# Optimization experiments

Hardware: AMD Instinct MI355X
Metric: run time of the kernel (lower is better)

## Reference

```python
import jax, jax.numpy as jnp
import numpy as np
import math

H = 2048; NH = 16; HD = 128; E = 8; K = 2; F = 8192; CAP_F = 1.25
B = 2; S = 2048

def _layernorm(x, scale, bias, eps=1e-5):
    m = jnp.mean(x, axis=-1, keepdims=True)
    v = jnp.var(x, axis=-1, keepdims=True)
    return (x - m) * jax.lax.rsqrt(v + eps) * scale + bias

def _rope(x):
    # x: [B, S, NH, HD]; half-split RoPE, theta=10000
    hd = x.shape[-1]
    pos = jnp.arange(x.shape[1], dtype=jnp.float32)
    freqs = 1.0 / (10000.0 ** (jnp.arange(0, hd // 2, dtype=jnp.float32) / (hd // 2)))
    ang = pos[:, None] * freqs[None, :]              # [S, HD/2]
    cos = jnp.cos(ang)[None, :, None, :]
    sin = jnp.sin(ang)[None, :, None, :]
    x1, x2 = jnp.split(x, 2, axis=-1)
    return jnp.concatenate([x1 * cos - x2 * sin, x1 * sin + x2 * cos], axis=-1)

def setup_inputs() -> dict:
    key = jax.random.key(0)
    ks = jax.random.split(key, 16)
    std = 0.02
    inp = {
        'hidden_states': jax.random.normal(ks[0], (B, S, H), jnp.float32),
        'attention_mask': jnp.ones((B, S), jnp.int32),
        'ln1_scale': jnp.ones((H,), jnp.float32), 'ln1_bias': jnp.zeros((H,), jnp.float32),
        'ln2_scale': jnp.ones((H,), jnp.float32), 'ln2_bias': jnp.zeros((H,), jnp.float32),
        'Wq': jax.random.normal(ks[1], (H, NH * HD), jnp.float32) * std,
        'Wk': jax.random.normal(ks[2], (H, NH * HD), jnp.float32) * std,
        'Wv': jax.random.normal(ks[3], (H, NH * HD), jnp.float32) * std,
        'Wo': jax.random.normal(ks[4], (NH * HD, H), jnp.float32) * std,
        'Wg': jax.random.normal(ks[5], (H, H), jnp.float32) * std,
        'bg': jnp.zeros((H,), jnp.float32),
        'ls_attn': jnp.full((H,), 0.1, jnp.float32),
        'ls_moe': jnp.full((H,), 0.1, jnp.float32),
        'router_w': jax.random.normal(ks[6], (H, E), jnp.float32) * std,
        'W1': jax.random.normal(ks[7], (E, H, F), jnp.float32) * std,
        'b1': jnp.zeros((E, F), jnp.float32),
        'W2': jax.random.normal(ks[8], (E, F, H), jnp.float32) * std,
        'b2': jnp.zeros((E, H), jnp.float32),
    }
    return inp

def _forward(hidden_states, attention_mask, ln1_scale, ln1_bias, ln2_scale, ln2_bias,
             Wq, Wk, Wv, Wo, Wg, bg, ls_attn, ls_moe, router_w, W1, b1, W2, b2):
    b, s, h = hidden_states.shape
    # ---- pre-norm MLA attention + residual ----
    xn = _layernorm(hidden_states, ln1_scale, ln1_bias)
    q = (xn @ Wq).reshape(b, s, NH, HD)
    k = (xn @ Wk).reshape(b, s, NH, HD)
    v = (xn @ Wv).reshape(b, s, NH, HD)
    q = _rope(q); k = _rope(k)
    scores = jnp.einsum('bqhd,bkhd->bhqk', q, k) / math.sqrt(HD)
    causal = jnp.tril(jnp.ones((s, s), bool))
    mask = causal[None, None, :, :] & (attention_mask[:, None, None, :] > 0)
    scores = jnp.where(mask, scores, -1e9)
    attn = jax.nn.softmax(scores, axis=-1)
    ctx = jnp.einsum('bhqk,bkhd->bqhd', attn, v).reshape(b, s, NH * HD)
    attn_out = ctx @ Wo
    attn_out = attn_out * jax.nn.sigmoid(xn @ Wg + bg)   # output gating
    attn_out = attn_out * ls_attn                         # layer scale
    hidden_states = hidden_states + attn_out
    # ---- pre-norm MoE FFN + residual ----
    xn2 = _layernorm(hidden_states, ln2_scale, ln2_bias)
    T = b * s
    x = xn2.reshape(T, h)
    logits = (x @ router_w).astype(jnp.float32)           # [T, E]
    probs = jax.nn.softmax(logits, axis=-1)
    gates, idx = jax.lax.top_k(probs, K)                  # [T, K]
    gates = gates / jnp.sum(gates, axis=-1, keepdims=True)
    cap = int(math.ceil(T * K / E * CAP_F))               # expert capacity
    e_flat = idx.reshape(T * K)
    g_flat = gates.reshape(T * K)
    oh = jax.nn.one_hot(e_flat, E, dtype=jnp.int32)       # [TK, E]
    pos = jnp.sum(jnp.cumsum(oh, axis=0) * oh, axis=-1) - 1
    keep = (pos < cap).astype(x.dtype)
    pos_c = jnp.clip(pos, 0, cap - 1)
    x_rep = jnp.repeat(x, K, axis=0)                      # [TK, H]
    buf = jnp.zeros((E, cap, h), x.dtype).at[e_flat, pos_c].add(x_rep * keep[:, None])
    hmid = jax.nn.gelu(jnp.einsum('ech,ehf->ecf', buf, W1) + b1[:, None, :])
    obuf = jnp.einsum('ecf,efh->ech', hmid, W2) + b2[:, None, :]
    tok = obuf[e_flat, pos_c] * (keep * g_flat)[:, None]  # [TK, H]
    moe_out = tok.reshape(T, K, h).sum(axis=1).reshape(b, s, h)
    moe_out = moe_out * ls_moe
    return hidden_states + moe_out

def reference(hidden_states, attention_mask, ln1_scale, ln1_bias, ln2_scale, ln2_bias,
              Wq, Wk, Wv, Wo, Wg, bg, ls_attn, ls_moe, router_w, W1, b1, W2, b2):
    return _forward(hidden_states, attention_mask, ln1_scale, ln1_bias, ln2_scale, ln2_bias,
                    Wq, Wk, Wv, Wo, Wg, bg, ls_attn, ls_moe, router_w, W1, b1, W2, b2)
```

## Files before the change

### kernel.cpp

```cpp
#include <hip/hip_runtime.h>
#include <hip/hip_fp16.h>

typedef _Float16 f16;
typedef _Float16 half8 __attribute__((ext_vector_type(8)));
typedef float floatx4 __attribute__((ext_vector_type(4)));

constexpr int kH  = 2048;
constexpr int kS  = 2048;
constexpr int kB  = 2;
constexpr int kT  = kB * kS;
constexpr int kNH = 16;
constexpr int kHD = 128;
constexpr int kE  = 8;
constexpr int kF  = 8192;
constexpr int kCAP = 1280;
constexpr int kTK = kT * 2;

__device__ __forceinline__ void gload16(const void* g, void* lds_) {
  __builtin_amdgcn_global_load_lds((const __attribute__((address_space(1))) void*)g,
                                   (__attribute__((address_space(3))) void*)lds_,
                                   16, 0, 0);
}

__global__ __launch_bounds__(256) void transpose_cvt(
    const float* __restrict__ src, f16* __restrict__ dst,
    int ldS, int ldD, long sZ, long dZ)
{
  __shared__ float tile[64][65];
  src += (long)blockIdx.z * sZ;
  dst += (long)blockIdx.z * dZ;
  const int kb = blockIdx.y * 64, nb = blockIdx.x * 64;
  const int tx = threadIdx.x & 15, ty = threadIdx.x >> 4;
#pragma unroll
  for (int i = 0; i < 4; i++) {
    const int r = ty + i * 16;
    const float4 v = *(const float4*)&src[(long)(kb + r) * ldS + nb + tx * 4];
    tile[r][tx * 4 + 0] = v.x; tile[r][tx * 4 + 1] = v.y;
    tile[r][tx * 4 + 2] = v.z; tile[r][tx * 4 + 3] = v.w;
  }
  __syncthreads();
#pragma unroll
  for (int i = 0; i < 4; i++) {
    const int n = ty + i * 16;
    union { f16 h[4]; unsigned long long u; } pk;
#pragma unroll
    for (int j = 0; j < 4; j++) pk.h[j] = (f16)tile[tx * 4 + j][n];
    *(unsigned long long*)&dst[(long)(nb + n) * ldD + kb + tx * 4] = pk.u;
  }
}

__global__ __launch_bounds__(256) void ln_kernel(
    const float* __restrict__ x, const float* __restrict__ sc,
    const float* __restrict__ bi, f16* __restrict__ o16, float* __restrict__ o32)
{
  const long row = blockIdx.x;
  const float* xr = x + row * kH;
  const int t = threadIdx.x;
  const float4 u = ((const float4*)xr)[t * 2];
  const float4 v = ((const float4*)xr)[t * 2 + 1];
  float s = u.x + u.y + u.z + u.w + v.x + v.y + v.z + v.w;
  float q = u.x*u.x + u.y*u.y + u.z*u.z + u.w*u.w + v.x*v.x + v.y*v.y + v.z*v.z + v.w*v.w;
#pragma unroll
  for (int m = 1; m < 64; m <<= 1) { s += __shfl_xor(s, m); q += __shfl_xor(q, m); }
  __shared__ float red_s[4], red_q[4];
  const int w = t >> 6, l = t & 63;
  if (l == 0) { red_s[w] = s; red_q[w] = q; }
  __syncthreads();
  s = red_s[0] + red_s[1] + red_s[2] + red_s[3];
  q = red_q[0] + red_q[1] + red_q[2] + red_q[3];
  const float mean = s * (1.f / kH);
  const float var = q * (1.f / kH) - mean * mean;
  const float rstd = rsqrtf(var + 1e-5f);
  const int c = t * 8;
  const float vals[8] = {u.x, u.y, u.z, u.w, v.x, v.y, v.z, v.w};
#pragma unroll
  for (int j = 0; j < 8; j++) {
    const float y = (vals[j] - mean) * rstd * sc[c + j] + bi[c + j];
    o16[row * kH + c + j] = (f16)y;
    if (o32 != nullptr) o32[row * kH + c + j] = y;
  }
}

template <int EPI>
__global__ __launch_bounds__(256) void gemm_kernel(
    const f16* __restrict__ A, const f16* __restrict__ B, void* __restrict__ Cv,
    const float* __restrict__ bias, const int* __restrict__ rowCount,
    int M, int N, int K, long aZ, long bZ, long cZ, long biasZ)
{
  const int z = blockIdx.z;
  if (rowCount != nullptr && (int)(blockIdx.y * 128) >= rowCount[z]) return;
  __shared__ f16 As[128 * 64];
  __shared__ f16 Bs[128 * 64];
  A += (long)z * aZ;  B += (long)z * bZ;
  const int tid = threadIdx.x, w = tid >> 6, l = tid & 63;
  const int g = l >> 4, lr = l & 15;
  const long m0 = (long)blockIdx.y * 128, n0 = (long)blockIdx.x * 128;
  const int wm = (w >> 1) * 64, wn = (w & 1) * 64;
  floatx4 acc[4][4];
#pragma unroll
  for (int i = 0; i < 4; i++)
#pragma unroll
    for (int j = 0; j < 4; j++) acc[i][j] = floatx4{0.f, 0.f, 0.f, 0.f};
  const int lrow = l >> 3, lwb = (l & 7) * 16;
  const int nk = K >> 6;
  for (int kt = 0; kt < nk; kt++) {
    const long k0 = (long)kt * 64;
#pragma unroll
    for (int c = 0; c < 4; c++) {
      const int rbase = w * 32 + c * 8;
      const int row = rbase + lrow;
      const int srcoff = (lwb ^ ((row & 7) << 4)) >> 1;
      gload16(A + (m0 + row) * K + k0 + srcoff, As + rbase * 64);
      gload16(B + (n0 + row) * K + k0 + srcoff, Bs + rbase * 64);
    }
    asm volatile("s_waitcnt vmcnt(0)" ::: "memory");
    __syncthreads();
#pragma unroll
    for (int kc = 0; kc < 2; kc++) {
      half8 af[4], bf[4];
#pragma unroll
      for (int i = 0; i < 4; i++) {
        const int ra = wm + i * 16 + lr;
        af[i] = *(const half8*)((const char*)As + ra * 128 + ((kc * 64 + g * 16) ^ ((ra & 7) << 4)));
        const int rb = wn + i * 16 + lr;
        bf[i] = *(const half8*)((const char*)Bs + rb * 128 + ((kc * 64 + g * 16) ^ ((rb & 7) << 4)));
      }
#pragma unroll
      for (int mi = 0; mi < 4; mi++)
#pragma unroll
        for (int ni = 0; ni < 4; ni++)
          acc[mi][ni] = __builtin_amdgcn_mfma_f32_16x16x32_f16(af[mi], bf[ni], acc[mi][ni], 0, 0, 0);
    }
    __syncthreads();
  }
  const long crow = m0 + wm + g * 4;
  const long ccol = n0 + wn + lr;
#pragma unroll
  for (int mi = 0; mi < 4; mi++)
#pragma unroll
    for (int ni = 0; ni < 4; ni++)
#pragma unroll
      for (int j = 0; j < 4; j++) {
        const long r = crow + mi * 16 + j;
        const long c = ccol + ni * 16;
        float v = acc[mi][ni][j];
        if (EPI == 0) {
          ((float*)Cv)[(long)z * cZ + r * N + c] = v;
        } else {
          v += bias[(long)z * biasZ + c];
          ((f16*)Cv)[(long)z * cZ + r * N + c] = (f16)v;
        }
      }
}

#define STG(SRC, TILE, KC, PAR, MAT) { \
  const f16* s_ = (SRC) + (long)(TILE) * 64 + (KC) * 32; \
  char* d_ = lds + ((PAR) * 65536 + (MAT) * 32768 + (KC) * 16384) + ldsW; \
  gload16(s_, d_); \
  gload16(s_ + 128 * ldGl, d_ + 8192); }

#define MROW(MH, MM, AF) \
  acc[(MH)*4+(MM)][0] = __builtin_amdgcn_mfma_f32_16x16x32_f16(AF, bf0, acc[(MH)*4+(MM)][0], 0, 0, 0); \
  acc[(MH)*4+(MM)][1] = __builtin_amdgcn_mfma_f32_16x16x32_f16(AF, bf1, acc[(MH)*4+(MM)][1], 0, 0, 0); \
  acc[(MH)*4+(MM)][2] = __builtin_amdgcn_mfma_f32_16x16x32_f16(AF, bf2, acc[(MH)*4+(MM)][2], 0, 0, 0); \
  acc[(MH)*4+(MM)][3] = __builtin_amdgcn_mfma_f32_16x16x32_f16(AF, bf3, acc[(MH)*4+(MM)][3], 0, 0, 0);

#define PH(PAR, KC, MH, RB, STAGE_STMT, VM_STMT) { \
  const char* au_ = lds + ((PAR) * 65536 + (KC) * 16384); \
  const char* bu_ = lds + ((PAR) * 65536 + 32768 + (KC) * 16384); \
  af0 = *(const half8*)(au_ + afoff + (MH) * 4096 +    0); \
  af1 = *(const half8*)(au_ + afoff + (MH) * 4096 + 1024); \
  af2 = *(const half8*)(au_ + afoff + (MH) * 4096 + 2048); \
  af3 = *(const half8*)(au_ + afoff + (MH) * 4096 + 3072); \
  if (RB) { \
    bf0 = *(const half8*)(bu_ + bfoff +    0); \
    bf1 = *(const half8*)(bu_ + bfoff + 1024); \
    bf2 = *(const half8*)(bu_ + bfoff + 2048); \
    bf3 = *(const half8*)(bu_ + bfoff + 3072); \
  } \
  STAGE_STMT; \
  VM_STMT; \
  __builtin_amdgcn_sched_barrier(0); \
  __builtin_amdgcn_s_barrier(); \
  asm volatile("s_waitcnt lgkmcnt(0)" ::: "memory"); \
  __builtin_amdgcn_sched_barrier(0); \
  __builtin_amdgcn_s_setprio(1); \
  MROW(MH, 0, af0) MROW(MH, 1, af1) MROW(MH, 2, af2) MROW(MH, 3, af3) \
  __builtin_amdgcn_s_setprio(0); }

#define VM6 asm volatile("s_waitcnt vmcnt(6)" ::: "memory")
#define VM0 asm volatile("s_waitcnt vmcnt(0)" ::: "memory")
#define NOP (void)0

template <int EPI, bool SPLITK>
__global__ __launch_bounds__(512, 2) void gemm8p_kernel(
    const f16* __restrict__ A, const f16* __restrict__ B, void* __restrict__ Cv,
    const float* __restrict__ bias, const int* __restrict__ rowCount,
    int M, int N, int K, long ldA, long ldB, long aZ, long bZ, long cZ,
    long cZ2, long biasZ)
{
  const int z = blockIdx.z;
  const int ze = SPLITK ? (z >> 1) : z;
  if (rowCount != nullptr && (int)(blockIdx.y * 256) >= rowCount[ze]) return;
  __shared__ __align__(16) char lds[131072];
  const long khoff = SPLITK ? (long)(z & 1) * K : 0;
  A += (long)ze * aZ + khoff;  B += (long)ze * bZ + khoff;
  const int tid = threadIdx.x, w = tid >> 6, l = tid & 63;
  const int g = l >> 4, lr = l & 15;
  const long m0 = (long)blockIdx.y * 256, n0 = (long)blockIdx.x * 256;
  const int wm = (w >> 2) * 128, wn = (w & 3) * 64;

  floatx4 acc[8][4];
#pragma unroll
  for (int i = 0; i < 8; i++)
#pragma unroll
    for (int j = 0; j < 4; j++) acc[i][j] = floatx4{0.f, 0.f, 0.f, 0.f};

  const int swzS = ((l & 3) * 8) ^ (((l >> 3) & 3) << 3);
  const f16* aSrc;
  const f16* bSrc;
  long ldGl;
  {
    const int srow = w * 16 + (l >> 2);
    aSrc = A + (m0 + srow) * ldA + swzS;
    bSrc = B + (n0 + srow) * ldB + swzS;
  }
  ldGl = ldA;
  const int ldsW = w * 1024;
  const int rsw = (g * 16) ^ (((lr >> 1) & 3) << 4);
  const int afoff = wm * 64 + lr * 64 + rsw;
  const int bfoff = wn * 64 + lr * 64 + rsw;
  half8 af0, af1, af2, af3;
  half8 bf0 = half8{0}, bf1 = half8{0}, bf2 = half8{0}, bf3 = half8{0};

  STG(aSrc, 0, 0, 0, 0);
  STG(bSrc, 0, 0, 0, 1);
  STG(aSrc, 0, 1, 0, 0);
  STG(bSrc, 0, 1, 0, 1);
  STG(bSrc, 1, 0, 1, 1);
  STG(aSrc, 1, 0, 1, 0);
  STG(bSrc, 1, 1, 1, 1);
  VM6;
  __builtin_amdgcn_sched_barrier(0);
  __builtin_amdgcn_s_barrier();

  const int NI = K >> 7;
  for (int i = 0; i < NI - 1; i++) {
    const int t0 = 2 * i, t1 = 2 * i + 1;
    PH(0, 0, 0, 1, STG(aSrc, (t1),     1, 1, 0), NOP)
    PH(0, 0, 1, 0, STG(bSrc, (t0 + 2), 0, 0, 1), NOP)
    PH(0, 1, 0, 1, STG(aSrc, (t0 + 2), 0, 0, 0), NOP)
    PH(0, 1, 1, 0, STG(bSrc, (t0 + 2), 1, 0, 1), VM6)
    PH(1, 0, 0, 1, STG(aSrc, (t0 + 2), 1, 0, 0), NOP)
    PH(1, 0, 1, 0, STG(bSrc, (t1 + 2), 0, 1, 1), NOP)
    PH(1, 1, 0, 1, STG(aSrc, (t1 + 2), 0, 1, 0), NOP)
    PH(1, 1, 1, 0, STG(bSrc, (t1 + 2), 1, 1, 1), VM6)
  }
  {
    const int t1 = 2 * (NI - 1) + 1;
    PH(0, 0, 0, 1, STG(aSrc, (t1), 1, 1, 0), NOP)
    PH(0, 0, 1, 0, NOP, NOP)
    PH(0, 1, 0, 1, NOP, NOP)
    PH(0, 1, 1, 0, NOP, VM0)
    PH(1, 0, 0, 1, NOP, NOP)
    PH(1, 0, 1, 0, NOP, NOP)
    PH(1, 1, 0, 1, NOP, NOP)
    PH(1, 1, 1, 0, NOP, NOP)
  }

  const long crow = m0 + wm + g * 4;
  const long ccol = n0 + wn + lr;
  float* c32 = (float*)Cv + (long)ze * cZ + (SPLITK ? (long)(z & 1) * cZ2 : 0);
#pragma unroll
  for (int mi = 0; mi < 8; mi++)
#pragma unroll
    for (int ni = 0; ni < 4; ni++)
#pragma unroll
      for (int j = 0; j < 4; j++) {
        const long r = crow + mi * 16 + j;
        const long c = ccol + ni * 16;
        float v = acc[mi][ni][j];
        if (EPI == 0) {
          c32[r * N + c] = v;
        } else if (EPI == 2) {
          v += bias[(long)ze * biasZ + c];
          const float u2 = 1.5957691216057308f * (v + 0.044715f * v * v * v);
          const float sg = 1.f / (1.f + __expf(-u2));
          ((f16*)Cv)[(long)ze * cZ + r * N + c] = (f16)(v * sg);
        } else {
          v += bias[(long)ze * biasZ + c];
          ((f16*)Cv)[(long)ze * cZ + r * N + c] = (f16)v;
        }
      }
}
#undef STG
#undef MROW
#undef PH
#undef VM6
#undef VM0
#undef NOP

__global__ void rope_table_kernel(float* __restrict__ ct, float* __restrict__ st) {
  const int i = blockIdx.x * 256 + threadIdx.x;
  if (i >= kS * 64) return;
  const int s = i >> 6, f = i & 63;
  const double freq = exp(-0.14391156831212787 * (double)f);
  const double ang = (double)s * freq;
  ct[i] = (float)cos(ang);
  st[i] = (float)sin(ang);
}

__global__ __launch_bounds__(256) void rope_kernel(
    const float* __restrict__ q, const float* __restrict__ k,
    const float* __restrict__ ct, const float* __restrict__ st,
    f16* __restrict__ qr, f16* __restrict__ kr)
{
  const long t = blockIdx.x;
  const int s = (int)(t & (kS - 1)), b = (int)(t >> 11);
  for (int u = threadIdx.x; u < kNH * 64; u += 256) {
    const int h = u >> 6, i = u & 63;
    const float c = ct[s * 64 + i], sn = st[s * 64 + i];
    const long src = t * kH + h * kHD + i;
    const long dst = (((long)(b * kNH + h)) * kS + s) * kHD + i;
    float x1 = q[src], x2 = q[src + 64];
    qr[dst]      = (f16)((x1 * c - x2 * sn) * 0.08838834764831845f);
    qr[dst + 64] = (f16)((x1 * sn + x2 * c) * 0.08838834764831845f);
    x1 = k[src]; x2 = k[src + 64];
    kr[dst]      = (f16)(x1 * c - x2 * sn);
    kr[dst + 64] = (f16)(x1 * sn + x2 * c);
  }
}

__global__ __launch_bounds__(256) void attn_kernel(
    const f16* __restrict__ q_r, const f16* __restrict__ k_r,
    const f16* __restrict__ v_t, f16* __restrict__ ctx)
{
  __shared__ f16 Ks[64 * 128];
  __shared__ f16 Vs[128 * 64];
  __shared__ f16 Ps[4][1024];
  const int qt = blockIdx.x, h = blockIdx.y, b = blockIdx.z;
  const int bh = b * kNH + h;
  const int tid = threadIdx.x, w = tid >> 6, l = tid & 63;
  const int g = l >> 4, lr = l & 15;
  const long q0 = (long)qt * 64;
  const f16* qbase = q_r + ((long)bh * kS + q0 + w * 16 + lr) * kHD;
  half8 qf[4];
#pragma unroll
  for (int kc = 0; kc < 4; kc++) qf[kc] = *(const half8*)(qbase + kc * 32 + g * 8);
  floatx4 acc[8];
#pragma unroll
  for (int i = 0; i < 8; i++) acc[i] = floatx4{0.f, 0.f, 0.f, 0.f};
  float mrun[4], lrun[4];
#pragma unroll
  for (int j = 0; j < 4; j++) { mrun[j] = -1e30f; lrun[j] = 0.f; }
  f16* pw = Ps[w];

  for (int kt = 0; kt <= qt; kt++) {
    const long k0 = (long)kt * 64;
#pragma unroll
    for (int c = 0; c < 4; c++) {
      const int cc = w * 4 + c;
      const int row = cc * 4 + (l >> 4);
      const int wb = (l & 15) * 16;
      const int src = (wb ^ ((row & 7) << 4)) >> 1;
      gload16(k_r + ((long)bh * kS + k0 + row) * kHD + src, Ks + cc * 512);
    }
#pragma unroll
    for (int c = 0; c < 4; c++) {
      const int cc = w * 4 + c;
      const int row = cc * 8 + (l >> 3);
      const int wb = (l & 7) * 16;
      const int src = (wb ^ ((row & 7) << 4)) >> 1;
      gload16(v_t + ((long)bh * kHD + row) * kS + k0 + src, Vs + cc * 512);
    }
    asm volatile("s_waitcnt vmcnt(0)" ::: "memory");
    __syncthreads();

    floatx4 sfr[4];
#pragma unroll
    for (int f = 0; f < 4; f++) {
      floatx4 s4 = floatx4{0.f, 0.f, 0.f, 0.f};
      const int row = f * 16 + lr;
#pragma unroll
      for (int kc = 0; kc < 4; kc++) {
        const half8 kfq = *(const half8*)((const char*)Ks + row * 256 +
                            ((kc * 64 + g * 16) ^ ((row & 7) << 4)));
        s4 = __builtin_amdgcn_mfma_f32_16x16x32_f16(qf[kc], kfq, s4, 0, 0, 0);
      }
      sfr[f] = s4;
    }
    if (kt == qt) {
#pragma unroll
      for (int f = 0; f < 4; f++) {
        const int key = kt * 64 + f * 16 + lr;
#pragma unroll
        for (int j = 0; j < 4; j++) {
          const int qrow = qt * 64 + w * 16 + g * 4 + j;
          if (key > qrow) sfr[f][j] = -1e30f;
        }
      }
    }
    float al[4];
#pragma unroll
    for (int j = 0; j < 4; j++) {
      float pm = fmaxf(fmaxf(sfr[0][j], sfr[1][j]), fmaxf(sfr[2][j], sfr[3][j]));
      pm = fmaxf(pm, __shfl_xor(pm, 1)); pm = fmaxf(pm, __shfl_xor(pm, 2));
      pm = fmaxf(pm, __shfl_xor(pm, 4)); pm = fmaxf(pm, __shfl_xor(pm, 8));
      const float mn = fmaxf(mrun[j], pm);
      al[j] = __expf(mrun[j] - mn);
      mrun[j] = mn;
      float rs = 0.f;
#pragma unroll
      for (int f = 0; f < 4; f++) {
        const float p = __expf(sfr[f][j] - mn);
        sfr[f][j] = p; rs += p;
      }
      rs += __shfl_xor(rs, 1); rs += __shfl_xor(rs, 2);
      rs += __shfl_xor(rs, 4); rs += __shfl_xor(rs, 8);
      lrun[j] = lrun[j] * al[j] + rs;
    }
#pragma unroll
    for (int nf = 0; nf < 8; nf++)
#pragma unroll
      for (int j = 0; j < 4; j++) acc[nf][j] *= al[j];
#pragma unroll
    for (int f = 0; f < 4; f++)
#pragma unroll
      for (int j = 0; j < 4; j++) {
        const int row = g * 4 + j;
        const int byteoff = (row * 128 + (f * 16 + lr) * 2) ^ ((row & 7) << 4);
        *(f16*)((char*)pw + byteoff) = (f16)sfr[f][j];
      }
#pragma unroll
    for (int kc = 0; kc < 2; kc++) {
      const half8 pf = *(const half8*)((const char*)pw + lr * 128 +
                         ((kc * 64 + g * 16) ^ ((lr & 7) << 4)));
#pragma unroll
      for (int nf = 0; nf < 8; nf++) {
        const int vrow = nf * 16 + lr;
        const half8 vfr = *(const half8*)((const char*)Vs + vrow * 128 +
                            ((kc * 64 + g * 16) ^ ((vrow & 7) << 4)));
        acc[nf] = __builtin_amdgcn_mfma_f32_16x16x32_f16(pf, vfr, acc[nf], 0, 0, 0);
      }
    }
    __syncthreads();
  }
  const long orow = (long)b * kS + q0 + w * 16;
#pragma unroll
  for (int j = 0; j < 4; j++) {
    const float inv = 1.0f / lrun[j];
    const int r = g * 4 + j;
#pragma unroll
    for (int nf = 0; nf < 8; nf++)
      ctx[(orow + r) * kH + h * kHD + nf * 16 + lr] = (f16)(acc[nf][j] * inv);
  }
}

__global__ __launch_bounds__(256) void combine1_kernel(
    const float* __restrict__ hid, const float* __restrict__ alin,
    const float* __restrict__ glin, const float* __restrict__ bg,
    const float* __restrict__ ls, float* __restrict__ out)
{
  const long i = (long)blockIdx.x * 256 + threadIdx.x;
  const float4 hv = ((const float4*)hid)[i];
  const float4 av = ((const float4*)alin)[i];
  const float4 gv = ((const float4*)glin)[i];
  const int c = (int)(i & 511);
  const float4 lv = ((const float4*)ls)[c];
  const float4 bv = ((const float4*)bg)[c];
  float4 o;
  o.x = hv.x + lv.x * av.x / (1.f + __expf(-(gv.x + bv.x)));
  o.y = hv.y + lv.y * av.y / (1.f + __expf(-(gv.y + bv.y)));
  o.z = hv.z + lv.z * av.z / (1.f + __expf(-(gv.z + bv.z)));
  o.w = hv.w + lv.w * av.w / (1.f + __expf(-(gv.w + bv.w)));
  ((float4*)out)[i] = o;
}

__global__ __launch_bounds__(256) void router_kernel(
    const float* __restrict__ x, const float* __restrict__ rw,
    int* __restrict__ eidx, float* __restrict__ gates)
{
  const int t = blockIdx.x * 4 + (threadIdx.x >> 6);
  const int l = threadIdx.x & 63;
  const float* xr = x + (long)t * kH;
  float a[8] = {0.f, 0.f, 0.f, 0.f, 0.f, 0.f, 0.f, 0.f};
  for (int it = 0; it < kH / 64; it++) {
    const float xv = xr[it * 64 + l];
    const float* r = rw + (long)(it * 64 + l) * kE;
#pragma unroll
    for (int e = 0; e < 8; e++) a[e] += xv * r[e];
  }
#pragma unroll
  for (int e = 0; e < 8; e++)
#pragma unroll
    for (int m = 1; m < 64; m <<= 1) a[e] += __shfl_xor(a[e], m);
  if (l == 0) {
    float mx = a[0];
#pragma unroll
    for (int e = 1; e < 8; e++) mx = fmaxf(mx, a[e]);
    float p[8];
#pragma unroll
    for (int e = 0; e < 8; e++) p[e] = __expf(a[e] - mx);
    int i1 = 0; float v1 = p[0];
#pragma unroll
    for (int e = 1; e < 8; e++) if (p[e] > v1) { v1 = p[e]; i1 = e; }
    int i2 = -1; float v2 = -1.f;
#pragma unroll
    for (int e = 0; e < 8; e++) if (e != i1 && p[e] > v2) { v2 = p[e]; i2 = e; }
    const float inv = 1.f / (v1 + v2);
    eidx[t * 2] = i1; eidx[t * 2 + 1] = i2;
    gates[t * 2] = v1 * inv; gates[t * 2 + 1] = v2 * inv;
  }
}

__global__ void scan_kernel(const int* __restrict__ eidx, int* __restrict__ slot,
                            int* __restrict__ counts)
{
  const int l = threadIdx.x;
  int base[8] = {0, 0, 0, 0, 0, 0, 0, 0};
  const unsigned long long lt = (1ull << l) - 1ull;
  for (int it = 0; it < kTK / 64; it++) {
    const int i = it * 64 + l;
    const int e = eidx[i];
    int mypos = 0;
#pragma unroll
    for (int ex = 0; ex < 8; ex++) {
      const unsigned long long mk = __ballot(e == ex);
      if (e == ex) mypos = base[ex] + __popcll(mk & lt);
      base[ex] += __popcll(mk);
    }
    slot[i] = (mypos < kCAP) ? e * kCAP + mypos : -1;
  }
  if (l == 0) {
#pragma unroll
    for (int ex = 0; ex < 8; ex++) counts[ex] = min(base[ex], kCAP);
  }
}

__global__ __launch_bounds__(256) void scatter_kernel(
    const f16* __restrict__ xh, const int* __restrict__ slot, f16* __restrict__ buf)
{
  const int i = blockIdx.x;
  const int s = slot[i];
  if (s < 0) return;
  const long t = i >> 1;
  ((half8*)(buf + (long)s * kH))[threadIdx.x] =
      ((const half8*)(xh + t * kH))[threadIdx.x];
}

__global__ __launch_bounds__(256) void combine2_kernel(
    const float* __restrict__ hid2, const float* __restrict__ P0,
    const float* __restrict__ P1, const int* __restrict__ slot,
    const float* __restrict__ gates, const float* __restrict__ b2,
    const float* __restrict__ ls, float* __restrict__ out)
{
  const int t = blockIdx.x;
  const int c = threadIdx.x * 8;
  float m[8] = {0.f, 0.f, 0.f, 0.f, 0.f, 0.f, 0.f, 0.f};
#pragma unroll
  for (int ks = 0; ks < 2; ks++) {
    const int s = slot[t * 2 + ks];
    if (s < 0) continue;
    const float gte = gates[t * 2 + ks];
    const int e = s / kCAP;
    const long ro = (long)s * kH + c;
    const float4 p0a = *(const float4*)&P0[ro];
    const float4 p0b = *(const float4*)&P0[ro + 4];
    const float4 p1a = *(const float4*)&P1[ro];
    const float4 p1b = *(const float4*)&P1[ro + 4];
    const float4 ba = *(const float4*)&b2[e * kH + c];
    const float4 bb = *(const float4*)&b2[e * kH + c + 4];
    m[0] += gte * (p0a.x + p1a.x + ba.x);
    m[1] += gte * (p0a.y + p1a.y + ba.y);
    m[2] += gte * (p0a.z + p1a.z + ba.z);
    m[3] += gte * (p0a.w + p1a.w + ba.w);
    m[4] += gte * (p0b.x + p1b.x + bb.x);
    m[5] += gte * (p0b.y + p1b.y + bb.y);
    m[6] += gte * (p0b.z + p1b.z + bb.z);
    m[7] += gte * (p0b.w + p1b.w + bb.w);
  }
  const float* hp = hid2 + (long)t * kH + c;
  float* op = out + (long)t * kH + c;
#pragma unroll
  for (int j = 0; j < 8; j++) op[j] = hp[j] + ls[c + j] * m[j];
}

extern "C" void kernel_launch(void* const* d_in, const int* in_sizes, int n_in,
                              void* d_out, int out_size, void* d_ws, size_t ws_size,
                              hipStream_t stream)
{
  (void)in_sizes; (void)n_in;
  const float* hidden   = (const float*)d_in[0];
  const float* ln1s     = (const float*)d_in[2];
  const float* ln1b     = (const float*)d_in[3];
  const float* ln2s     = (const float*)d_in[4];
  const float* ln2b     = (const float*)d_in[5];
  const float* Wq       = (const float*)d_in[6];
  const float* Wk       = (const float*)d_in[7];
  const float* Wv       = (const float*)d_in[8];
  const float* Wo       = (const float*)d_in[9];
  const float* Wg       = (const float*)d_in[10];
  const float* bg       = (const float*)d_in[11];
  const float* ls_attn  = (const float*)d_in[12];
  const float* ls_moe   = (const float*)d_in[13];
  const float* router_w = (const float*)d_in[14];
  const float* W1       = (const float*)d_in[15];
  const float* b1       = (const float*)d_in[16];
  const float* W2       = (const float*)d_in[17];
  const float* b2       = (const float*)d_in[18];

  char* ws = (char*)d_ws;
  size_t off = 0;
  auto take = [&](size_t b) { size_t r = off; off += (b + 255) & ~(size_t)255; return r; };
  const size_t o_wT   = take(5ULL * kH * kH * 2);
  const size_t o_w1t  = take((size_t)kE * kF * kH * 2);
  const size_t o_w2t  = take((size_t)kE * kH * kF * 2);
  const size_t o_xn   = take((size_t)kT * kH * 2);
  const size_t o_qkvg = take(4ULL * kT * kH * 4);
  const size_t o_tab  = take(2ULL * kS * 64 * 4);
  const size_t o_qr   = take(3ULL * kT * kH * 2);
  const size_t o_ctx  = take((size_t)kT * kH * 2);
  const size_t o_h2   = take((size_t)kT * kH * 4);
  const size_t o_sm   = take(1 << 20);
  const size_t o_hmid = take((size_t)kE * kCAP * kF * 2);
  if (off > ws_size) { hipMemsetAsync(d_out, 0xFF, (size_t)out_size * 4, stream); return; }

  f16* wT    = (f16*)(ws + o_wT);
  f16* w1t   = (f16*)(ws + o_w1t);
  f16* w2t   = (f16*)(ws + o_w2t);
  f16* xn    = (f16*)(ws + o_xn);
  float* qf  = (float*)(ws + o_qkvg);
  float* kfp = qf + (size_t)kT * kH;
  float* vfp = kfp + (size_t)kT * kH;
  float* gfp = vfp + (size_t)kT * kH;
  float* tabc = (float*)(ws + o_tab);
  float* tabs = tabc + (size_t)kS * 64;
  f16* qr  = (f16*)(ws + o_qr);
  f16* kr  = qr + (size_t)kT * kH;
  f16* vt  = kr + (size_t)kT * kH;
  f16* ctx = (f16*)(ws + o_ctx);
  float* h2 = (float*)(ws + o_h2);
  int* eidx    = (int*)(ws + o_sm);
  float* gates = (float*)(ws + o_sm + 65536);
  int* slot    = (int*)(ws + o_sm + 131072);
  int* counts  = (int*)(ws + o_sm + 196608);
  f16* hmid = (f16*)(ws + o_hmid);
  float* attn_lin = qf;
  float* x2f = vfp;
  f16* x2h  = (f16*)(ws + o_qkvg + 1ULL * kT * kH * 4 + (size_t)kT * kH * 2);
  f16* buf  = qr;
  float* P0 = (float*)(ws + o_qkvg);
  float* P1 = (float*)(ws + o_w1t);
  const long pStride = (long)(P1 - P0);

  const long HH = (long)kH * kH;

  transpose_cvt<<<dim3(32, 32, 1), 256, 0, stream>>>(Wq, wT + 0 * HH, kH, kH, 0, 0);
  transpose_cvt<<<dim3(32, 32, 1), 256, 0, stream>>>(Wk, wT + 1 * HH, kH, kH, 0, 0);
  transpose_cvt<<<dim3(32, 32, 1), 256, 0, stream>>>(Wv, wT + 2 * HH, kH, kH, 0, 0);
  transpose_cvt<<<dim3(32, 32, 1), 256, 0, stream>>>(Wg, wT + 3 * HH, kH, kH, 0, 0);
  transpose_cvt<<<dim3(32, 32, 1), 256, 0, stream>>>(Wo, wT + 4 * HH, kH, kH, 0, 0);
  transpose_cvt<<<dim3(kF / 64, kH / 64, kE), 256, 0, stream>>>(
      W1, w1t, kF, kH, (long)kH * kF, (long)kF * kH);
  transpose_cvt<<<dim3(kH / 64, kF / 64, kE), 256, 0, stream>>>(
      W2, w2t, kH, kF, (long)kF * kH, (long)kH * kF);
  ln_kernel<<<kT, 256, 0, stream>>>(hidden, ln1s, ln1b, xn, nullptr);
  gemm8p_kernel<0, false><<<dim3(kH / 256, kT / 256, 4), 512, 0, stream>>>(
      xn, wT, qf, nullptr, nullptr, kT, kH, kH, kH, kH,
      0L, HH, (long)kT * kH, 0L, 0L);
  rope_table_kernel<<<(kS * 64 + 255) / 256, 256, 0, stream>>>(tabc, tabs);
  rope_kernel<<<kT, 256, 0, stream>>>(qf, kfp, tabc, tabs, qr, kr);
  for (int b = 0; b < kB; b++)
    transpose_cvt<<<dim3(kHD / 64, kS / 64, kNH), 256, 0, stream>>>(
        vfp + (size_t)b * kS * kH, vt + (size_t)b * kNH * kHD * kS,
        kH, kS, 128L, (long)kHD * kS);
  attn_kernel<<<dim3(kS / 64, kNH, kB), 256, 0, stream>>>(qr, kr, vt, ctx);
  gemm_kernel<0><<<dim3(kH / 128, kT / 128, 1), 256, 0, stream>>>(
      ctx, wT + 4 * HH, attn_lin, nullptr, nullptr, kT, kH, kH, 0L, 0L, 0L, 0L);
  combine1_kernel<<<(kT * kH / 4) / 256, 256, 0, stream>>>(
      hidden, attn_lin, gfp, bg, ls_attn, h2);
  ln_kernel<<<kT, 256, 0, stream>>>(h2, ln2s, ln2b, x2h, x2f);
  router_kernel<<<kT / 4, 256, 0, stream>>>(x2f, router_w, eidx, gates);
  scan_kernel<<<1, 64, 0, stream>>>(eidx, slot, counts);
  scatter_kernel<<<kTK, 256, 0, stream>>>(x2h, slot, buf);
  gemm8p_kernel<2, false><<<dim3(kF / 256, kCAP / 256, kE), 512, 0, stream>>>(
      buf, w1t, hmid, b1, counts, kCAP, kF, kH, kH, kH,
      (long)kCAP * kH, (long)kF * kH, (long)kCAP * kF, 0L, (long)kF);
  gemm8p_kernel<0, true><<<dim3(kH / 256, kCAP / 256, 2 * kE), 512, 0, stream>>>(
      hmid, w2t, P0, nullptr, counts, kCAP, kH, 4096, kF, kF,
      (long)kCAP * kF, (long)kH * kF, (long)kCAP * kH, pStride, 0L);
  combine2_kernel<<<kT, 256, 0, stream>>>(
      h2, P0, P1, slot, gates, b2, ls_moe, (float*)d_out);
}
```

Before: 1.692 ms.

## Add XCD-aware block remapping and finer-grained vmcnt waits in GEMM pipeline

Adds an xcd_remap helper that renumbers workgroups so consecutive logical tiles land on the same XCD, and applies it to the GEMM and attention kernels to improve L2 locality. The GEMM main loop swaps the coarse per-half vmcnt(6) waits for a vmcnt(10) wait in every phase, with a retuned drain in the tail. The intent is to keep more global->LDS loads in flight and to cut cache misses across XCDs. The remap assumes the total grid is divisible by 8, and the new wait counts must match the exact load issue order or stale LDS data could be read.

After: 1.635 ms. 1.04x faster.

```diff
diff --git a/kernel.cpp b/kernel.cpp
--- a/kernel.cpp
+++ b/kernel.cpp
@@ -20,6 +20,16 @@
   __builtin_amdgcn_global_load_lds((const __attribute__((address_space(1))) void*)g,
                                    (__attribute__((address_space(3))) void*)lds_,
                                    16, 0, 0);
+}
+
+__device__ __forceinline__ void xcd_remap(int& bx, int& by, int& bz) {
+  const int gx = gridDim.x, gy = gridDim.y;
+  const int nwg = gx * gy * gridDim.z;
+  int L = (bz * gy + by) * gx + bx;
+  L = (L & 7) * (nwg >> 3) + (L >> 3);
+  bz = L / (gx * gy);
+  const int r = L - bz * gx * gy;
+  by = r / gx;  bx = r - by * gx;
 }
 
 __global__ __launch_bounds__(256) void transpose_cvt(
@@ -188,8 +198,10 @@
   MROW(MH, 0, af0) MROW(MH, 1, af1) MROW(MH, 2, af2) MROW(MH, 3, af3) \
   __builtin_amdgcn_s_setprio(0); }
 
-#define VM6 asm volatile("s_waitcnt vmcnt(6)" ::: "memory")
-#define VM0 asm volatile("s_waitcnt vmcnt(0)" ::: "memory")
+#define VM10 asm volatile("s_waitcnt vmcnt(10)" ::: "memory")
+#define VM8  asm volatile("s_waitcnt vmcnt(8)" ::: "memory")
+#define VM4  asm volatile("s_waitcnt vmcnt(4)" ::: "memory")
+#define VM0  asm volatile("s_waitcnt vmcnt(0)" ::: "memory")
 #define NOP (void)0
 
 template <int EPI, bool SPLITK>
@@ -199,15 +211,17 @@
     int M, int N, int K, long ldA, long ldB, long aZ, long bZ, long cZ,
     long cZ2, long biasZ)
 {
-  const int z = blockIdx.z;
+  int bx = blockIdx.x, by = blockIdx.y, bz = blockIdx.z;
+  xcd_remap(bx, by, bz);
+  const int z = bz;
   const int ze = SPLITK ? (z >> 1) : z;
-  if (rowCount != nullptr && (int)(blockIdx.y * 256) >= rowCount[ze]) return;
+  if (rowCount != nullptr && (int)(by * 256) >= rowCount[ze]) return;
   __shared__ __align__(16) char lds[131072];
   const long khoff = SPLITK ? (long)(z & 1) * K : 0;
   A += (long)ze * aZ + khoff;  B += (long)ze * bZ + khoff;
   const int tid = threadIdx.x, w = tid >> 6, l = tid & 63;
   const int g = l >> 4, lr = l & 15;
-  const long m0 = (long)blockIdx.y * 256, n0 = (long)blockIdx.x * 256;
+  const long m0 = (long)by * 256, n0 = (long)bx * 256;
   const int wm = (w >> 2) * 128, wn = (w & 3) * 64;
 
   floatx4 acc[8][4];
@@ -240,29 +254,29 @@
   STG(bSrc, 1, 0, 1, 1);
   STG(aSrc, 1, 0, 1, 0);
   STG(bSrc, 1, 1, 1, 1);
-  VM6;
+  VM10;
   __builtin_amdgcn_sched_barrier(0);
   __builtin_amdgcn_s_barrier();
 
   const int NI = K >> 7;
   for (int i = 0; i < NI - 1; i++) {
     const int t0 = 2 * i, t1 = 2 * i + 1;
-    PH(0, 0, 0, 1, STG(aSrc, (t1),     1, 1, 0), NOP)
-    PH(0, 0, 1, 0, STG(bSrc, (t0 + 2), 0, 0, 1), NOP)
-    PH(0, 1, 0, 1, STG(aSrc, (t0 + 2), 0, 0, 0), NOP)
-    PH(0, 1, 1, 0, STG(bSrc, (t0 + 2), 1, 0, 1), VM6)
-    PH(1, 0, 0, 1, STG(aSrc, (t0 + 2), 1, 0, 0), NOP)
-    PH(1, 0, 1, 0, STG(bSrc, (t1 + 2), 0, 1, 1), NOP)
-    PH(1, 1, 0, 1, STG(aSrc, (t1 + 2), 0, 1, 0), NOP)
-    PH(1, 1, 1, 0, STG(bSrc, (t1 + 2), 1, 1, 1), VM6)
+    PH(0, 0, 0, 1, STG(aSrc, (t1),     1, 1, 0), VM10)
+    PH(0, 0, 1, 0, STG(bSrc, (t0 + 2), 0, 0, 1), VM10)
+    PH(0, 1, 0, 1, STG(aSrc, (t0 + 2), 0, 0, 0), VM10)
+    PH(0, 1, 1, 0, STG(bSrc, (t0 + 2), 1, 0, 1), VM10)
+    PH(1, 0, 0, 1, STG(aSrc, (t0 + 2), 1, 0, 0), VM10)
+    PH(1, 0, 1, 0, STG(bSrc, (t1 + 2), 0, 1, 1), VM10)
+    PH(1, 1, 0, 1, STG(aSrc, (t1 + 2), 0, 1, 0), VM10)
+    PH(1, 1, 1, 0, STG(bSrc, (t1 + 2), 1, 1, 1), VM10)
   }
   {
     const int t1 = 2 * (NI - 1) + 1;
-    PH(0, 0, 0, 1, STG(aSrc, (t1), 1, 1, 0), NOP)
+    PH(0, 0, 0, 1, STG(aSrc, (t1), 1, 1, 0), VM8)
     PH(0, 0, 1, 0, NOP, NOP)
-    PH(0, 1, 0, 1, NOP, NOP)
-    PH(0, 1, 1, 0, NOP, VM0)
-    PH(1, 0, 0, 1, NOP, NOP)
+    PH(0, 1, 0, 1, NOP, VM4)
+    PH(0, 1, 1, 0, NOP, NOP)
+    PH(1, 0, 0, 1, NOP, VM0)
     PH(1, 0, 1, 0, NOP, NOP)
     PH(1, 1, 0, 1, NOP, NOP)
     PH(1, 1, 1, 0, NOP, NOP)
@@ -296,7 +310,9 @@
 #undef STG
 #undef MROW
 #undef PH
-#undef VM6
+#undef VM10
+#undef VM8
+#undef VM4
 #undef VM0
 #undef NOP
 
@@ -338,7 +354,8 @@
   __shared__ f16 Ks[64 * 128];
   __shared__ f16 Vs[128 * 64];
   __shared__ f16 Ps[4][1024];
-  const int qt = blockIdx.x, h = blockIdx.y, b = blockIdx.z;
+  int qt = blockIdx.x, h = blockIdx.y, b = blockIdx.z;
+  xcd_remap(qt, h, b);
   const int bh = b * kNH + h;
   const int tid = threadIdx.x, w = tid >> 6, l = tid & 63;
   const int g = l >> 4, lr = l & 15;
```
